# Optimization experiments

Measured on AMD Instinct MI355X. Metric: run time of the kernel, lower is better.

Reference implementation:

```python
import jax, jax.numpy as jnp
import numpy as np

DIM = 1024
NUM_HEADS = 16
HEAD_DIM = DIM // NUM_HEADS
SCALE = HEAD_DIM ** -0.5


def setup_inputs() -> dict:
    key = jax.random.key(0)
    ks = jax.random.split(key, 10)
    B, N, C = 8, 2048, DIM
    std = C ** -0.5
    return {
        "query": jax.random.normal(ks[0], (B, N, C), jnp.float32),
        "key": jax.random.normal(ks[1], (B, N, C), jnp.float32),
        "value": jax.random.normal(ks[2], (B, N, C), jnp.float32),
        "xpos": jax.random.randint(ks[3], (B, N, 2), 0, 64),
        "ypos": jax.random.randint(ks[4], (B, N, 2), 0, 64),
        # Linear weights stored [out, in] like torch; qkv_bias=False so no q/k/v bias.
        "Wq": jax.random.normal(ks[5], (C, C), jnp.float32) * std,
        "Wk": jax.random.normal(ks[6], (C, C), jnp.float32) * std,
        "Wv": jax.random.normal(ks[7], (C, C), jnp.float32) * std,
        "Wp": jax.random.normal(ks[8], (C, C), jnp.float32) * std,
        "bp": jax.random.normal(ks[9], (C,), jnp.float32) * std,
    }


def reference(query, key, value, xpos, ypos, Wq, Wk, Wv, Wp, bp):
    B, N, C = query.shape
    H, D = NUM_HEADS, HEAD_DIM
    # Separate Q/K/V projections (no bias), reshape to (B, N, H, D).
    q = (query @ Wq.T).reshape(B, N, H, D)
    k = (key @ Wk.T).reshape(B, N, H, D)
    v = (value @ Wv.T).reshape(B, N, H, D)
    # rope is None in this config, so no rotary embedding is applied.
    # Faithful to the source: NO permute before q @ k^T, so the contraction is
    # over D with attention logits of shape (B, N, H, H) (softmax over heads).
    attn = jnp.einsum("bnhd,bngd->bnhg", q, k) * SCALE
    attn = jax.nn.softmax(attn, axis=-1)
    x = jnp.einsum("bnhg,bngd->bnhd", attn, v)  # (B, N, H, D)
    # torch: (attn @ v).transpose(1, 2).reshape(B, N, C)
    x = jnp.transpose(x, (0, 2, 1, 3)).reshape(B, N, C)
    # Output projection (has bias); dropouts are p=0 / eval -> identity.
    return x @ Wp.T + bp
```

## Files before the change

kernel.cpp:

```cpp
#include <hip/hip_runtime.h>
#include <stdint.h>

#define DEV __device__ __forceinline__

using f32x4 = __attribute__((ext_vector_type(4))) float;
using s16x8 = __attribute__((ext_vector_type(8))) short;

DEV uint16_t f2bf(float f) {
  union { float f; uint32_t u; } v; v.f = f;
  uint32_t r = v.u + 0x7fffu + ((v.u >> 16) & 1u);
  return (uint16_t)(r >> 16);
}
DEV uint32_t pack2(float a, float b) {
  return (uint32_t)f2bf(a) | ((uint32_t)f2bf(b) << 16);
}

DEV void gload_lds16(const void* g, void* l) {
  __builtin_amdgcn_global_load_lds(
      (__attribute__((address_space(1))) void*)(void*)g,
      (__attribute__((address_space(3))) void*)l, 16, 0, 0);
}

__global__ __launch_bounds__(256) void cvt_all_kernel(
    const float* __restrict__ q, const float* __restrict__ k,
    const float* __restrict__ v, const float* __restrict__ Wq,
    const float* __restrict__ Wk, const float* __restrict__ Wv,
    const float* __restrict__ Wp, uint16_t* __restrict__ qc,
    uint16_t* __restrict__ kc, uint16_t* __restrict__ vc,
    uint16_t* __restrict__ wqb, uint16_t* __restrict__ wkb,
    uint16_t* __restrict__ wvb, uint16_t* __restrict__ wpb) {
  const int idx = blockIdx.x * blockDim.x + threadIdx.x;
  const float* src;
  uint16_t* dst;
  int i;
  if (idx < 3 * 2097152) {
    const int t = idx >> 21;
    i = idx & 2097151;
    src = t == 0 ? q : t == 1 ? k : v;
    dst = t == 0 ? qc : t == 1 ? kc : vc;
  } else {
    const int j = idx - 3 * 2097152;
    const int r = j >> 17;
    i = j & 131071;
    src = r == 0 ? Wq : r == 1 ? Wk : r == 2 ? Wv : Wp;
    dst = r == 0 ? wqb : r == 1 ? wkb : r == 2 ? wvb : wpb;
  }
  const float4* s = (const float4*)src;
  float4 a = s[2 * i];
  float4 b = s[2 * i + 1];
  uint4 pk;
  pk.x = pack2(a.x, a.y);
  pk.y = pack2(a.z, a.w);
  pk.z = pack2(b.x, b.y);
  pk.w = pack2(b.z, b.w);
  ((uint4*)dst)[i] = pk;
}

struct GemmBatch {
  const uint16_t* A[3];
  const uint16_t* B[3];
  void* C[3];
};

template <bool OUT_BF16>
__global__ __launch_bounds__(512, 2) void gemm8p(GemmBatch gb,
                                                 const float* __restrict__ bias,
                                                 int M, int N, int K) {
  constexpr int BM = 256, BN = 256, BK = 64;
  __shared__ __align__(16) uint16_t Alds[2][BM * BK];
  __shared__ __align__(16) uint16_t Blds[2][BN * BK];

  const int w = blockIdx.x;
  const int xcd = w & 7;
  int local = w >> 3;
  const int nbn = N >> 8;
  const int bmpx = (M >> 8) >> 3;
  const int bn = local % nbn;
  local /= nbn;
  const int bml = local % bmpx;
  const int z = local / bmpx;
  const int bm0 = (xcd * bmpx + bml) * BM;
  const int bn0 = bn * BN;

  const uint16_t* __restrict__ Ap = gb.A[z];
  const uint16_t* __restrict__ Bp = gb.B[z];
  void* __restrict__ Cp = gb.C[z];

  const int tid = threadIdx.x;
  const int wave = tid >> 6;
  const int lane = tid & 63;
  const int quad = lane >> 4;
  const int l16 = lane & 15;
  const int wm = (wave >> 2) * 128;
  const int wn = (wave & 3) * 64;

  f32x4 acc[8][4];
#pragma unroll
  for (int i = 0; i < 8; ++i)
#pragma unroll
    for (int j = 0; j < 4; ++j) acc[i][j] = (f32x4){0.f, 0.f, 0.f, 0.f};

  size_t aofs[2][2], bofs[2][2];
  int lofs[2][2];
#pragma unroll
  for (int h = 0; h < 2; ++h)
#pragma unroll
    for (int j = 0; j < 2; ++j) {
      const int p = h * 1024 + wave * 128 + j * 64 + lane;
      const int m = p >> 3;
      const int lc = (p & 7) ^ ((m >> 1) & 7);
      aofs[h][j] = (size_t)(bm0 + m) * K + lc * 8;
      bofs[h][j] = (size_t)(bn0 + m) * K + lc * 8;
      lofs[h][j] = (h * 1024 + wave * 128 + j * 64) * 8;
    }

  auto SA = [&](int tile, int h) {
    uint16_t* base = Alds[tile & 1];
#pragma unroll
    for (int j = 0; j < 2; ++j)
      gload_lds16(Ap + aofs[h][j] + (size_t)tile * BK, base + lofs[h][j]);
  };
  auto SB = [&](int tile, int h) {
    uint16_t* base = Blds[tile & 1];
#pragma unroll
    for (int j = 0; j < 2; ++j)
      gload_lds16(Bp + bofs[h][j] + (size_t)tile * BK, base + lofs[h][j]);
  };

  s16x8 Af[4][2], Bf[4][2];
  auto LDA = [&](int buf, int mh) {
#pragma unroll
    for (int s = 0; s < 4; ++s) {
      const int ml = wm + (mh * 4 + s) * 16 + l16;
      const int sw = (ml >> 1) & 7;
#pragma unroll
      for (int k = 0; k < 2; ++k) {
        const int cc = ml * 8 + ((k * 4 + quad) ^ sw);
        Af[s][k] = *(const s16x8*)&Alds[buf][cc * 8];
      }
    }
  };
  auto LDB = [&](int buf, int nh) {
#pragma unroll
    for (int s = 0; s < 2; ++s) {
      const int nl = wn + (nh * 2 + s) * 16 + l16;
      const int sw = (nl >> 1) & 7;
#pragma unroll
      for (int k = 0; k < 2; ++k) {
        const int cc = nl * 8 + ((k * 4 + quad) ^ sw);
        Bf[nh * 2 + s][k] = *(const s16x8*)&Blds[buf][cc * 8];
      }
    }
  };
  auto OPEN = [&]() {
    __builtin_amdgcn_s_barrier();
    asm volatile("s_waitcnt lgkmcnt(0)" ::: "memory");
    __builtin_amdgcn_sched_barrier(0);
  };
  auto MMA = [&](int mh, int nh) {
    __builtin_amdgcn_s_setprio(1);
#pragma unroll
    for (int s = 0; s < 4; ++s)
#pragma unroll
      for (int n = 0; n < 2; ++n)
#pragma unroll
        for (int k = 0; k < 2; ++k)
          acc[mh * 4 + s][nh * 2 + n] = __builtin_amdgcn_mfma_f32_16x16x32_bf16(
              Af[s][k], Bf[nh * 2 + n][k], acc[mh * 4 + s][nh * 2 + n], 0, 0, 0);
    __builtin_amdgcn_s_setprio(0);
  };
  auto CLOSE = [&]() { __builtin_amdgcn_s_barrier(); };

  const int NT = K >> 6;
  const int NI = NT >> 1;

  SA(0, 0); SA(0, 1); SB(0, 0); SB(0, 1); SB(1, 0); SB(1, 1);
  asm volatile("s_waitcnt vmcnt(4)" ::: "memory");
  __builtin_amdgcn_s_barrier();

  for (int i = 0; i < NI; ++i) {
    const int t0 = 2 * i, t1 = 2 * i + 1;
    const bool more = (t0 + 2 < NT);

    LDA(0, 0); LDB(0, 0);
    SA(t1, 0);
    OPEN(); MMA(0, 0); CLOSE();
    LDB(0, 1);
    SA(t1, 1);
    OPEN(); MMA(0, 1); CLOSE();
    LDA(0, 1);
    if (more) SB(t0 + 2, 0);
    OPEN(); MMA(1, 0); CLOSE();
    if (more) SB(t0 + 2, 1);
    OPEN(); MMA(1, 1);
    if (more) asm volatile("s_waitcnt vmcnt(4)" ::: "memory");
    else      asm volatile("s_waitcnt vmcnt(0)" ::: "memory");
    CLOSE();

    LDA(1, 0); LDB(1, 0);
    if (more) SA(t0 + 2, 0);
    OPEN(); MMA(0, 0); CLOSE();
    LDB(1, 1);
    if (more) SA(t0 + 2, 1);
    OPEN(); MMA(0, 1); CLOSE();
    LDA(1, 1);
    if (more) SB(t1 + 2, 0);
    OPEN(); MMA(1, 0); CLOSE();
    if (more) SB(t1 + 2, 1);
    OPEN(); MMA(1, 1);
    asm volatile("s_waitcnt vmcnt(4)" ::: "memory");
    CLOSE();
  }

#pragma unroll
  for (int sm = 0; sm < 8; ++sm) {
    const int mrow = bm0 + wm + sm * 16 + quad * 4;
#pragma unroll
    for (int sn = 0; sn < 4; ++sn) {
      const int ncol = bn0 + wn + sn * 16 + l16;
      if constexpr (OUT_BF16) {
        uint16_t* Cb = (uint16_t*)Cp;
#pragma unroll
        for (int r = 0; r < 4; ++r) Cb[(size_t)(mrow + r) * N + ncol] = f2bf(acc[sm][sn][r]);
      } else {
        float* Cf = (float*)Cp;
        const float bv = bias[ncol];
#pragma unroll
        for (int r = 0; r < 4; ++r) Cf[(size_t)(mrow + r) * N + ncol] = acc[sm][sn][r] + bv;
      }
    }
  }
}

__global__ __launch_bounds__(256) void attn_kernel(const uint16_t* __restrict__ qb,
                                                   const uint16_t* __restrict__ kb,
                                                   const uint16_t* __restrict__ vb,
                                                   uint16_t* __restrict__ x2b) {
  __shared__ __align__(16) uint16_t plds[4][16 * 16];
  __shared__ __align__(16) uint16_t vlds[4][16 * 64];

  const int tid = threadIdx.x;
  const int wave = tid >> 6;
  const int lane = tid & 63;
  const int quad = lane >> 4;
  const int l16 = lane & 15;
  const int token = blockIdx.x * 4 + wave;
  const int b = token >> 11;
  const int n = token & 2047;
  const size_t base = (size_t)token * 1024;

  {
    const uint16_t* vt = vb + base;
    uint16_t* vl = vlds[wave];
#pragma unroll
    for (int c2 = 0; c2 < 2; ++c2) {
      const int p = lane + c2 * 64;
      const int g = p >> 3;
      const int cc = p & 7;
      const int cs = cc ^ (2 * (g >> 3));
      *(uint4*)&vl[g * 64 + cs * 8] = *(const uint4*)&vt[p * 8];
    }
  }

  const uint16_t* qrow = qb + base + l16 * 64 + quad * 8;
  const uint16_t* krow = kb + base + l16 * 64 + quad * 8;
  s16x8 aq0 = *(const s16x8*)qrow;
  s16x8 aq1 = *(const s16x8*)(qrow + 32);
  s16x8 bk0 = *(const s16x8*)krow;
  s16x8 bk1 = *(const s16x8*)(krow + 32);
  f32x4 s = (f32x4){0.f, 0.f, 0.f, 0.f};
  s = __builtin_amdgcn_mfma_f32_16x16x32_bf16(aq0, bk0, s, 0, 0, 0);
  s = __builtin_amdgcn_mfma_f32_16x16x32_bf16(aq1, bk1, s, 0, 0, 0);

  float p[4];
#pragma unroll
  for (int r = 0; r < 4; ++r) {
    float v = s[r] * 0.125f;
    float mx = v;
#pragma unroll
    for (int off = 1; off < 16; off <<= 1) mx = fmaxf(mx, __shfl_xor(mx, off));
    float e = __expf(v - mx);
    float sum = e;
#pragma unroll
    for (int off = 1; off < 16; off <<= 1) sum += __shfl_xor(sum, off);
    p[r] = e / sum;
  }

  uint16_t* pb = plds[wave];
#pragma unroll
  for (int r = 0; r < 4; ++r) pb[(quad * 4 + r) * 16 + l16] = f2bf(p[r]);
  __syncthreads();
  s16x8 ap = (s16x8){0, 0, 0, 0, 0, 0, 0, 0};
  if (quad < 2) ap = *(const s16x8*)&pb[l16 * 16 + quad * 8];

  s16x8 bv[4];
#pragma unroll
  for (int c = 0; c < 4; ++c) bv[c] = (s16x8){0, 0, 0, 0, 0, 0, 0, 0};
  if (quad < 2) {
    const uint16_t* vl = vlds[wave];
#pragma unroll
    for (int c = 0; c < 4; ++c) {
      const int cc = c * 2 + (l16 >> 3);
      const int dlo = l16 & 7;
#pragma unroll
      for (int j = 0; j < 8; ++j) {
        const int g = quad * 8 + j;
        const int cs = cc ^ (2 * (g >> 3));
        bv[c][j] = (short)vl[g * 64 + cs * 8 + dlo];
      }
    }
  }

  f32x4 xacc[4];
#pragma unroll
  for (int c = 0; c < 4; ++c) {
    xacc[c] = (f32x4){0.f, 0.f, 0.f, 0.f};
    xacc[c] = __builtin_amdgcn_mfma_f32_16x16x32_bf16(ap, bv[c], xacc[c], 0, 0, 0);
  }

  uint16_t* xout =
      x2b + (size_t)b * (2048 * 1024) + (size_t)(n & 15) * 64 + (size_t)(n >> 4) * 1024;
#pragma unroll
  for (int c = 0; c < 4; ++c) {
    const int d = c * 16 + l16;
#pragma unroll
    for (int r = 0; r < 4; ++r) {
      const int h = quad * 4 + r;
      xout[(size_t)h * 128 * 1024 + d] = f2bf(xacc[c][r]);
    }
  }
}

extern "C" void kernel_launch(void* const* d_in, const int* in_sizes, int n_in,
                              void* d_out, int out_size, void* d_ws, size_t ws_size,
                              hipStream_t stream) {
  const float* query = (const float*)d_in[0];
  const float* key = (const float*)d_in[1];
  const float* value = (const float*)d_in[2];
  const float* Wq = (const float*)d_in[5];
  const float* Wk = (const float*)d_in[6];
  const float* Wv = (const float*)d_in[7];
  const float* Wp = (const float*)d_in[8];
  const float* bp = (const float*)d_in[9];
  float* out = (float*)d_out;

  const int C = 1024;
  const int M = 8 * 2048;
  const size_t MC = (size_t)M * C;
  const size_t CC = (size_t)C * C;

  uint16_t* ws = (uint16_t*)d_ws;
  uint16_t* qb = ws;
  uint16_t* kb = qb + MC;
  uint16_t* vb = kb + MC;
  uint16_t* x2b = vb + MC;
  uint16_t* wqb = x2b + MC;
  uint16_t* wkb = wqb + CC;
  uint16_t* wvb = wkb + CC;
  uint16_t* wpb = wvb + CC;
  uint16_t* kin = wpb + CC;
  uint16_t* vin = kin + MC;
  uint16_t* qin = x2b;

  cvt_all_kernel<<<dim3(26624), dim3(256), 0, stream>>>(
      query, key, value, Wq, Wk, Wv, Wp, qin, kin, vin, wqb, wkb, wvb, wpb);

  GemmBatch qkv;
  qkv.A[0] = qin;  qkv.B[0] = wqb;  qkv.C[0] = qb;
  qkv.A[1] = kin;  qkv.B[1] = wkb;  qkv.C[1] = kb;
  qkv.A[2] = vin;  qkv.B[2] = wvb;  qkv.C[2] = vb;
  gemm8p<true><<<dim3((M / 256) * (C / 256) * 3), dim3(512), 0, stream>>>(qkv, nullptr,
                                                                          M, C, C);

  attn_kernel<<<dim3(M / 4), dim3(256), 0, stream>>>(qb, kb, vb, x2b);

  GemmBatch fin;
  fin.A[0] = x2b;  fin.B[0] = wpb;  fin.C[0] = out;
  fin.A[1] = x2b;  fin.B[1] = wpb;  fin.C[1] = out;
  fin.A[2] = x2b;  fin.B[2] = wpb;  fin.C[2] = out;
  gemm8p<false><<<dim3((M / 256) * (C / 256)), dim3(512), 0, stream>>>(fin, bp, M, C, C);
}
```

Measured before the change: 392.4 us.

## Load GEMM B operand straight from global into registers and triple-buffer A

```diff
diff --git a/kernel.cpp b/kernel.cpp
--- a/kernel.cpp
+++ b/kernel.cpp
@@ -66,9 +66,8 @@
 __global__ __launch_bounds__(512, 2) void gemm8p(GemmBatch gb,
                                                  const float* __restrict__ bias,
                                                  int M, int N, int K) {
-  constexpr int BM = 256, BN = 256, BK = 64;
-  __shared__ __align__(16) uint16_t Alds[2][BM * BK];
-  __shared__ __align__(16) uint16_t Blds[2][BN * BK];
+  constexpr int BM = 256, BK = 64;
+  __shared__ __align__(16) uint16_t Alds[3][BM * BK];
 
   const int w = blockIdx.x;
   const int xcd = w & 7;
@@ -80,7 +79,7 @@
   const int bml = local % bmpx;
   const int z = local / bmpx;
   const int bm0 = (xcd * bmpx + bml) * BM;
-  const int bn0 = bn * BN;
+  const int bn0 = bn * 256;
 
   const uint16_t* __restrict__ Ap = gb.A[z];
   const uint16_t* __restrict__ Bp = gb.B[z];
@@ -100,7 +99,7 @@
 #pragma unroll
     for (int j = 0; j < 4; ++j) acc[i][j] = (f32x4){0.f, 0.f, 0.f, 0.f};
 
-  size_t aofs[2][2], bofs[2][2];
+  size_t aofs[2][2];
   int lofs[2][2];
 #pragma unroll
   for (int h = 0; h < 2; ++h)
@@ -110,45 +109,31 @@
       const int m = p >> 3;
       const int lc = (p & 7) ^ ((m >> 1) & 7);
       aofs[h][j] = (size_t)(bm0 + m) * K + lc * 8;
-      bofs[h][j] = (size_t)(bn0 + m) * K + lc * 8;
       lofs[h][j] = (h * 1024 + wave * 128 + j * 64) * 8;
     }
 
   auto SA = [&](int tile, int h) {
-    uint16_t* base = Alds[tile & 1];
+    uint16_t* base = Alds[tile % 3];
 #pragma unroll
     for (int j = 0; j < 2; ++j)
       gload_lds16(Ap + aofs[h][j] + (size_t)tile * BK, base + lofs[h][j]);
   };
-  auto SB = [&](int tile, int h) {
-    uint16_t* base = Blds[tile & 1];
-#pragma unroll
-    for (int j = 0; j < 2; ++j)
-      gload_lds16(Bp + bofs[h][j] + (size_t)tile * BK, base + lofs[h][j]);
-  };
-
-  s16x8 Af[4][2], Bf[4][2];
-  auto LDA = [&](int buf, int mh) {
-#pragma unroll
-    for (int s = 0; s < 4; ++s) {
-      const int ml = wm + (mh * 4 + s) * 16 + l16;
+
+  const uint16_t* Brow[4];
+#pragma unroll
+  for (int s = 0; s < 4; ++s)
+    Brow[s] = Bp + (size_t)(bn0 + wn + s * 16 + l16) * K + quad * 8;
+
+  s16x8 Af[2][2], Bf[4][2];
+  auto LDA2 = [&](int buf, int q) {
+#pragma unroll
+    for (int s = 0; s < 2; ++s) {
+      const int ml = wm + (q * 2 + s) * 16 + l16;
       const int sw = (ml >> 1) & 7;
 #pragma unroll
       for (int k = 0; k < 2; ++k) {
         const int cc = ml * 8 + ((k * 4 + quad) ^ sw);
         Af[s][k] = *(const s16x8*)&Alds[buf][cc * 8];
-      }
-    }
-  };
-  auto LDB = [&](int buf, int nh) {
-#pragma unroll
-    for (int s = 0; s < 2; ++s) {
-      const int nl = wn + (nh * 2 + s) * 16 + l16;
-      const int sw = (nl >> 1) & 7;
-#pragma unroll
-      for (int k = 0; k < 2; ++k) {
-        const int cc = nl * 8 + ((k * 4 + quad) ^ sw);
-        Bf[nh * 2 + s][k] = *(const s16x8*)&Blds[buf][cc * 8];
       }
     }
   };
@@ -157,58 +142,48 @@
     asm volatile("s_waitcnt lgkmcnt(0)" ::: "memory");
     __builtin_amdgcn_sched_barrier(0);
   };
-  auto MMA = [&](int mh, int nh) {
+  auto MMA2 = [&](int q) {
     __builtin_amdgcn_s_setprio(1);
 #pragma unroll
-    for (int s = 0; s < 4; ++s)
-#pragma unroll
-      for (int n = 0; n < 2; ++n)
+    for (int s = 0; s < 2; ++s)
+#pragma unroll
+      for (int n = 0; n < 4; ++n)
 #pragma unroll
         for (int k = 0; k < 2; ++k)
-          acc[mh * 4 + s][nh * 2 + n] = __builtin_amdgcn_mfma_f32_16x16x32_bf16(
-              Af[s][k], Bf[nh * 2 + n][k], acc[mh * 4 + s][nh * 2 + n], 0, 0, 0);
+          acc[q * 2 + s][n] = __builtin_amdgcn_mfma_f32_16x16x32_bf16(
+              Af[s][k], Bf[n][k], acc[q * 2 + s][n], 0, 0, 0);
     __builtin_amdgcn_s_setprio(0);
   };
   auto CLOSE = [&]() { __builtin_amdgcn_s_barrier(); };
 
   const int NT = K >> 6;
-  const int NI = NT >> 1;
-
-  SA(0, 0); SA(0, 1); SB(0, 0); SB(0, 1); SB(1, 0); SB(1, 1);
+
+  SA(0, 0); SA(0, 1); SA(1, 0); SA(1, 1);
   asm volatile("s_waitcnt vmcnt(4)" ::: "memory");
   __builtin_amdgcn_s_barrier();
 
-  for (int i = 0; i < NI; ++i) {
-    const int t0 = 2 * i, t1 = 2 * i + 1;
-    const bool more = (t0 + 2 < NT);
-
-    LDA(0, 0); LDB(0, 0);
-    SA(t1, 0);
-    OPEN(); MMA(0, 0); CLOSE();
-    LDB(0, 1);
-    SA(t1, 1);
-    OPEN(); MMA(0, 1); CLOSE();
-    LDA(0, 1);
-    if (more) SB(t0 + 2, 0);
-    OPEN(); MMA(1, 0); CLOSE();
-    if (more) SB(t0 + 2, 1);
-    OPEN(); MMA(1, 1);
+  for (int t = 0; t < NT; ++t) {
+    const int buf = t % 3;
+    const bool more = (t + 2 < NT);
+
+#pragma unroll
+    for (int s = 0; s < 4; ++s)
+#pragma unroll
+      for (int k = 0; k < 2; ++k)
+        Bf[s][k] = *(const s16x8*)(Brow[s] + (size_t)t * BK + k * 32);
+
+    LDA2(buf, 0);
+    if (more) SA(t + 2, 0);
+    OPEN(); MMA2(0); CLOSE();
+    LDA2(buf, 1);
+    if (more) SA(t + 2, 1);
+    OPEN(); MMA2(1); CLOSE();
+    LDA2(buf, 2);
+    OPEN(); MMA2(2); CLOSE();
+    LDA2(buf, 3);
+    OPEN(); MMA2(3);
     if (more) asm volatile("s_waitcnt vmcnt(4)" ::: "memory");
     else      asm volatile("s_waitcnt vmcnt(0)" ::: "memory");
-    CLOSE();
-
-    LDA(1, 0); LDB(1, 0);
-    if (more) SA(t0 + 2, 0);
-    OPEN(); MMA(0, 0); CLOSE();
-    LDB(1, 1);
-    if (more) SA(t0 + 2, 1);
-    OPEN(); MMA(0, 1); CLOSE();
-    LDA(1, 1);
-    if (more) SB(t1 + 2, 0);
-    OPEN(); MMA(1, 0); CLOSE();
-    if (more) SB(t1 + 2, 1);
-    OPEN(); MMA(1, 1);
-    asm volatile("s_waitcnt vmcnt(4)" ::: "memory");
     CLOSE();
   }
 
@@ -289,7 +264,8 @@
   uint16_t* pb = plds[wave];
 #pragma unroll
   for (int r = 0; r < 4; ++r) pb[(quad * 4 + r) * 16 + l16] = f2bf(p[r]);
-  __syncthreads();
+  asm volatile("s_waitcnt lgkmcnt(0)" ::: "memory");
+  __builtin_amdgcn_sched_barrier(0);
   s16x8 ap = (s16x8){0, 0, 0, 0, 0, 0, 0, 0};
   if (quad < 2) ap = *(const s16x8*)&pb[l16 * 16 + quad * 8];
 
```

Result: slower. 495.3 us (+26.2%).
